# Optimization experiments

Measured on AMD Instinct MI355X. Metric: run time of the kernel, lower is better.

The kernel has to match this reference:

```python
import jax, jax.numpy as jnp
import numpy as np

VOCAB_SIZE = 4096
D_EMBED = 256
BETA = 0.25  # unused: module returns raw commit_loss; beta applied by caller


def setup_inputs() -> dict:
    key = jax.random.key(0)
    k_h, k_e = jax.random.split(key)
    h = jax.random.normal(k_h, (16, D_EMBED, 32, 32), dtype=jnp.float32)
    embedding = jax.random.normal(k_e, (VOCAB_SIZE, D_EMBED), dtype=jnp.float32)
    return {"h": h, "embedding": embedding}


def reference(h, embedding):
    B, C, H, W = h.shape
    h = h.astype(jnp.float32)
    # (B, C, H, W) -> (N, C) with N = B*H*W
    h_flat = jnp.transpose(h, (0, 2, 3, 1)).reshape(-1, C)
    dist = (
        jnp.sum(h_flat * h_flat, axis=1, keepdims=True)
        + jnp.sum(embedding * embedding, axis=1)
        - 2.0 * jnp.einsum("nc,vc->nv", h_flat, embedding)
    )
    indices_flat = jnp.argmin(dist, axis=1)
    indices = indices_flat.reshape(B, H, W)
    # gather codebook vectors and restore (B, C, H, W)
    z_q = jnp.transpose(embedding[indices_flat].reshape(B, H, W, C), (0, 3, 1, 2))
    commit_loss = jnp.mean((h - jax.lax.stop_gradient(z_q)) ** 2)
    # straight-through estimator
    z_q_st = h + jax.lax.stop_gradient(z_q - h)
    return z_q_st, indices, commit_loss
```

## Files before the change

kernel.cpp:

```cpp
#include <hip/hip_runtime.h>

#define D 256
#define VOCAB 4096
#define NTOT 16384
#define N_OUT0 4194304
#define MARGIN 0.95f

typedef _Float16 half8 __attribute__((ext_vector_type(8)));
typedef float f32x4 __attribute__((ext_vector_type(4)));

__device__ __forceinline__ void gld16(const void* g, void* l) {
    __builtin_amdgcn_global_load_lds(
        (const __attribute__((address_space(1))) void*)g,
        (__attribute__((address_space(3))) void*)l, 16, 0, 0);
}

__device__ __forceinline__ unsigned long long pack_key(float d, int v) {
    unsigned u = __float_as_uint(d);
    u ^= ((unsigned)((int)u >> 31)) | 0x80000000u;
    return ((unsigned long long)u << 32) | (unsigned)v;
}

__global__ __launch_bounds__(256) void k_pack(const float* __restrict__ h,
                                              const float* __restrict__ emb,
                                              _Float16* __restrict__ Apk,
                                              _Float16* __restrict__ Bpk,
                                              float* __restrict__ esq) {
    __shared__ float S[16384];
    const int tid = threadIdx.x;
    const int bid = blockIdx.x;
    if (bid < 256) {
        const int bm = bid >> 2, w = bid & 3;
        const int b = bm >> 2, p0 = (bm & 3) << 8;
#pragma unroll 4
        for (int cl = 0; cl < 64; ++cl)
            S[cl * 256 + tid] =
                h[((size_t)b << 18) + ((size_t)(w * 64 + cl) << 10) + (size_t)(p0 + tid)];
        __syncthreads();
        _Float16* dstA = Apk + (size_t)bm * 65536 + (size_t)w * 16384;
#pragma unroll
        for (int kk = 0; kk < 2; ++kk)
#pragma unroll
            for (int q = 0; q < 4; ++q) {
                alignas(16) _Float16 hv[8];
#pragma unroll
                for (int j = 0; j < 8; ++j) hv[j] = (_Float16)S[(kk * 32 + q * 8 + j) * 256 + tid];
                *(half8*)(dstA + (kk * 4 + q) * 2048 + tid * 8) = *(half8*)hv;
            }
    } else {
        const int bn = bid - 256, v0 = bn << 7;
        float eacc = 0.f;
        _Float16* dstB = Bpk + (size_t)bn * 32768;
        const int kk = tid >> 7, r = tid & 127;
        const int sr = (r & 64) + ((r & 15) * 4) + ((r & 63) >> 4);
        for (int w = 0; w < 4; ++w) {
            __syncthreads();
#pragma unroll 4
            for (int i = 0; i < 32; ++i) {
                int rr = i * 4 + (tid >> 6), cc = tid & 63;
                S[rr * 65 + cc] = emb[(size_t)(v0 + rr) * 256 + w * 64 + cc];
            }
            __syncthreads();
            if (tid < 128)
#pragma unroll 4
                for (int cc = 0; cc < 64; ++cc) { float x = S[tid * 65 + cc]; eacc = fmaf(x, x, eacc); }
#pragma unroll
            for (int q = 0; q < 4; ++q) {
                alignas(16) _Float16 ev[8];
#pragma unroll
                for (int j = 0; j < 8; ++j) ev[j] = (_Float16)S[sr * 65 + kk * 32 + q * 8 + j];
                *(half8*)(dstB + w * 8192 + (kk * 4 + q) * 1024 + r * 8) = *(half8*)ev;
            }
        }
        if (tid < 128) esq[v0 + tid] = eacc;
    }
}

__global__ __launch_bounds__(256, 2) void k_gemm(const _Float16* __restrict__ Apk,
                                                 const _Float16* __restrict__ Bpk,
                                                 const float* __restrict__ esq,
                                                 float* __restrict__ top1) {
    __shared__ _Float16 As[16384];
    __shared__ _Float16 Bs[8192];

    const int tid = threadIdx.x;
    const int bn = blockIdx.x >> 6, bm = blockIdx.x & 63;
    const int m0 = bm << 8, n0 = bn << 7;
    const int wv = tid >> 6, l = tid & 63;
    const int wm = wv & 1, wn = wv >> 1;
    const int quad = l >> 4, j16 = l & 15;

    f32x4 acc[8][4];
#pragma unroll
    for (int i = 0; i < 8; ++i)
#pragma unroll
        for (int j = 0; j < 4; ++j) acc[i][j] = (f32x4)0.0f;

    const char* Ag = (const char*)(Apk + (size_t)bm * 65536) + tid * 16;
    const char* Bg = (const char*)(Bpk + (size_t)bn * 32768) + tid * 16;
    _Float16* Asw = As + tid * 8;
    _Float16* Bsw = Bs + tid * 8;
    const _Float16* aB = As + quad * 2048 + (wm * 128 + j16) * 8;
    const _Float16* bB = Bs + quad * 1024 + (wn * 64 + j16) * 8;

    for (int w = 0; w < 4; ++w) {
#pragma unroll
        for (int i = 0; i < 8; ++i) gld16(Ag + w * 32768 + i * 4096, Asw + i * 2048);
#pragma unroll
        for (int i = 0; i < 4; ++i) gld16(Bg + w * 16384 + i * 4096, Bsw + i * 2048);
        __syncthreads();
#pragma unroll
        for (int kk = 0; kk < 2; ++kk) {
            half8 af[8], bf[4];
#pragma unroll
            for (int mt = 0; mt < 8; ++mt) af[mt] = *(const half8*)(aB + kk * 8192 + mt * 128);
#pragma unroll
            for (int nt = 0; nt < 4; ++nt) bf[nt] = *(const half8*)(bB + kk * 4096 + nt * 128);
#pragma unroll
            for (int mt = 0; mt < 8; ++mt)
#pragma unroll
                for (int nt = 0; nt < 4; ++nt)
                    acc[mt][nt] = __builtin_amdgcn_mfma_f32_16x16x32_f16(af[mt], bf[nt], acc[mt][nt], 0, 0, 0);
        }
        __syncthreads();
    }

    const float4 es4 = *(const float4*)(esq + n0 + wn * 64 + j16 * 4);
    const size_t tbase = ((size_t)m0 + wm * 128) * 128 + (unsigned)(bn * 4 + wn * 2 + (j16 >> 3));
#pragma unroll
    for (int mt = 0; mt < 8; ++mt) {
#pragma unroll
        for (int r = 0; r < 4; ++r) {
            float d0 = es4.x - 2.0f * acc[mt][0][r];
            float d1 = es4.y - 2.0f * acc[mt][1][r];
            float d2 = es4.z - 2.0f * acc[mt][2][r];
            float d3 = es4.w - 2.0f * acc[mt][3][r];
            float mn = fminf(fminf(d0, d1), fminf(d2, d3));
            mn = fminf(mn, __shfl_xor(mn, 1, 64));
            mn = fminf(mn, __shfl_xor(mn, 2, 64));
            mn = fminf(mn, __shfl_xor(mn, 4, 64));
            if ((j16 & 7) == 0)
                top1[tbase + (size_t)(mt * 16 + quad * 4 + r) * 128] = mn;
        }
    }
}

__global__ __launch_bounds__(256) void k_refine(const float* __restrict__ h,
                                                const float* __restrict__ emb,
                                                const float* __restrict__ esq,
                                                const float* __restrict__ top1,
                                                unsigned long long* __restrict__ gbest) {
    const int tid = threadIdx.x;
    const int n = blockIdx.x * 4 + (tid >> 6);
    const int l = tid & 63;
    const int b = n >> 10, p = n & 1023;

    const float2 gm = *(const float2*)(top1 + (size_t)n * 128 + l * 2);
    float m1 = fminf(gm.x, gm.y);
#pragma unroll
    for (int m = 32; m >= 1; m >>= 1) m1 = fminf(m1, __shfl_xor(m1, m, 64));
    const float thr = m1 + MARGIN;

    float hreg[4];
#pragma unroll
    for (int i = 0; i < 4; ++i)
        hreg[i] = h[((size_t)b << 18) + ((size_t)(l * 4 + i) << 10) + (size_t)p];

    unsigned long long best = ~0ULL;
#pragma unroll
    for (int j = 0; j < 2; ++j) {
        unsigned long long mask = __ballot((j == 0 ? gm.x : gm.y) <= thr);
        while (mask) {
            const int s = __builtin_ctzll(mask);
            mask &= mask - 1;
            const int g = s * 2 + j;
            const int vg = g << 5;
            for (int t = 0; t < 32; ++t) {
                const int v = vg + t;
                float4 e4 = *(const float4*)(emb + ((size_t)v << 8) + l * 4);
                float part = hreg[0] * e4.x;
                part = fmaf(hreg[1], e4.y, part);
                part = fmaf(hreg[2], e4.z, part);
                part = fmaf(hreg[3], e4.w, part);
#pragma unroll
                for (int m = 32; m >= 1; m >>= 1) part += __shfl_xor(part, m, 64);
                unsigned long long ke = pack_key(esq[v] - 2.0f * part, v);
                best = ke < best ? ke : best;
            }
        }
    }
    if (l == 0) gbest[n] = best;
}

__global__ __launch_bounds__(256) void k_gather(const float* __restrict__ h,
                                                const float* __restrict__ emb,
                                                const unsigned long long* __restrict__ gbest,
                                                float* __restrict__ out0,
                                                float* __restrict__ out1,
                                                float* __restrict__ plsum) {
    __shared__ float zq[32][260];
    __shared__ float wred[4];
    const int tid = threadIdx.x;
    const int lane = tid & 63;
    const int w = tid >> 6;
    const int n0 = blockIdx.x * 32;
    const int b = n0 >> 10;
    const int p0 = n0 & 1023;
#pragma unroll
    for (int rr = 0; rr < 8; ++rr) {
        int r = w * 8 + rr;
        unsigned idx = (unsigned)(gbest[n0 + r] & 0xFFFFFFFFULL);
        float4 e4 = *(const float4*)(emb + (size_t)idx * D + lane * 4);
        *(float4*)&zq[r][lane * 4] = e4;
    }
    if (tid < 32) {
        unsigned idx = (unsigned)(gbest[n0 + tid] & 0xFFFFFFFFULL);
        out1[n0 + tid] = (float)idx;
    }
    __syncthreads();
    float lsum = 0.0f;
    const size_t base = ((size_t)b * D) << 10;
#pragma unroll 4
    for (int it = 0; it < 32; ++it) {
        int c = it * 8 + (tid >> 5);
        int pp = tid & 31;
        float z = zq[pp][c];
        size_t g = base + ((size_t)c << 10) + p0 + pp;
        float hv = h[g];
        out0[g] = hv + (z - hv);
        float d = hv - z;
        lsum = fmaf(d, d, lsum);
    }
#pragma unroll
    for (int m = 32; m >= 1; m >>= 1) lsum += __shfl_xor(lsum, m, 64);
    if (lane == 0) wred[w] = lsum;
    __syncthreads();
    if (tid == 0) plsum[blockIdx.x] = wred[0] + wred[1] + wred[2] + wred[3];
}

__global__ __launch_bounds__(256) void k_fin(const float* __restrict__ plsum,
                                             float* __restrict__ out2) {
    __shared__ float wred[4];
    const int tid = threadIdx.x;
    float s = plsum[tid] + plsum[tid + 256];
#pragma unroll
    for (int m = 32; m >= 1; m >>= 1) s += __shfl_xor(s, m, 64);
    if ((tid & 63) == 0) wred[tid >> 6] = s;
    __syncthreads();
    if (tid == 0) out2[0] = (wred[0] + wred[1] + wred[2] + wred[3]) * (1.0f / (float)N_OUT0);
}

extern "C" void kernel_launch(void* const* d_in, const int* in_sizes, int n_in,
                              void* d_out, int out_size, void* d_ws, size_t ws_size,
                              hipStream_t stream) {
    const float* h = (const float*)d_in[0];
    const float* emb = (const float*)d_in[1];
    float* out0 = (float*)d_out;
    float* out1 = out0 + N_OUT0;
    float* out2 = out1 + NTOT;

    char* w = (char*)d_ws;
    _Float16* Apk = (_Float16*)(w);
    _Float16* Bpk = (_Float16*)(w + 8388608);
    float* top1 = (float*)(w + 10485760);
    float* esq = (float*)(w + 18874368);
    unsigned long long* gbest = (unsigned long long*)(w + 18890752);
    float* plsum = (float*)(w + 19021824);

    hipLaunchKernelGGL(k_pack, dim3(288), dim3(256), 0, stream, h, emb, Apk, Bpk, esq);
    hipLaunchKernelGGL(k_gemm, dim3(2048), dim3(256), 0, stream, Apk, Bpk, esq, top1);
    hipLaunchKernelGGL(k_refine, dim3(4096), dim3(256), 0, stream, h, emb, esq, top1, gbest);
    hipLaunchKernelGGL(k_gather, dim3(NTOT / 32), dim3(256), 0, stream, h, emb, gbest, out0, out1, plsum);
    hipLaunchKernelGGL(k_fin, dim3(1), dim3(256), 0, stream, plsum, out2);
}
```

Baseline: 210.1 us.

## Fuse refine and gather kernels, staging h tile in shared memory

Merges the per-row candidate refinement kernel and the gather/loss kernel into one kernel per 32-position block. The h tile is loaded once into shared memory, reused for the refinement dot products and for the output and loss pass, and the chosen indices stay in shared memory instead of going through a global buffer. This removes a launch, the gbest round-trip and a second strided read of h. The cost is that each block now runs 8 refine rows serially per wave with only 512 blocks, which lowers parallelism for the latency-bound refine loop.

Measured after the change: 244.0 us. +16.1%, slower.

```diff
diff --git a/kernel.cpp b/kernel.cpp
--- a/kernel.cpp
+++ b/kernel.cpp
@@ -145,89 +145,97 @@
     }
 }
 
-__global__ __launch_bounds__(256) void k_refine(const float* __restrict__ h,
+__global__ __launch_bounds__(256) void k_finish(const float* __restrict__ h,
                                                 const float* __restrict__ emb,
                                                 const float* __restrict__ esq,
                                                 const float* __restrict__ top1,
-                                                unsigned long long* __restrict__ gbest) {
-    const int tid = threadIdx.x;
-    const int n = blockIdx.x * 4 + (tid >> 6);
-    const int l = tid & 63;
-    const int b = n >> 10, p = n & 1023;
-
-    const float2 gm = *(const float2*)(top1 + (size_t)n * 128 + l * 2);
-    float m1 = fminf(gm.x, gm.y);
-#pragma unroll
-    for (int m = 32; m >= 1; m >>= 1) m1 = fminf(m1, __shfl_xor(m1, m, 64));
-    const float thr = m1 + MARGIN;
-
-    float hreg[4];
-#pragma unroll
-    for (int i = 0; i < 4; ++i)
-        hreg[i] = h[((size_t)b << 18) + ((size_t)(l * 4 + i) << 10) + (size_t)p];
-
-    unsigned long long best = ~0ULL;
-#pragma unroll
-    for (int j = 0; j < 2; ++j) {
-        unsigned long long mask = __ballot((j == 0 ? gm.x : gm.y) <= thr);
-        while (mask) {
-            const int s = __builtin_ctzll(mask);
-            mask &= mask - 1;
-            const int g = s * 2 + j;
-            const int vg = g << 5;
-            for (int t = 0; t < 32; ++t) {
-                const int v = vg + t;
-                float4 e4 = *(const float4*)(emb + ((size_t)v << 8) + l * 4);
-                float part = hreg[0] * e4.x;
-                part = fmaf(hreg[1], e4.y, part);
-                part = fmaf(hreg[2], e4.z, part);
-                part = fmaf(hreg[3], e4.w, part);
-#pragma unroll
-                for (int m = 32; m >= 1; m >>= 1) part += __shfl_xor(part, m, 64);
-                unsigned long long ke = pack_key(esq[v] - 2.0f * part, v);
-                best = ke < best ? ke : best;
-            }
-        }
-    }
-    if (l == 0) gbest[n] = best;
-}
-
-__global__ __launch_bounds__(256) void k_gather(const float* __restrict__ h,
-                                                const float* __restrict__ emb,
-                                                const unsigned long long* __restrict__ gbest,
                                                 float* __restrict__ out0,
                                                 float* __restrict__ out1,
                                                 float* __restrict__ plsum) {
+    __shared__ float Sh[32][257];
     __shared__ float zq[32][260];
+    __shared__ int idxs[32];
     __shared__ float wred[4];
+
     const int tid = threadIdx.x;
     const int lane = tid & 63;
     const int w = tid >> 6;
     const int n0 = blockIdx.x * 32;
     const int b = n0 >> 10;
     const int p0 = n0 & 1023;
+    const size_t base = (size_t)b << 18;
+
+    {
+        const int pp = tid & 31, c0 = tid >> 5;
+#pragma unroll 4
+        for (int it = 0; it < 32; ++it) {
+            int c = it * 8 + c0;
+            Sh[pp][c] = h[base + ((size_t)c << 10) + (size_t)(p0 + pp)];
+        }
+    }
+    __syncthreads();
+
+#pragma unroll 1
+    for (int rr = 0; rr < 8; ++rr) {
+        const int r = w * 8 + rr;
+        const int n = n0 + r;
+        const float2 gm = *(const float2*)(top1 + ((size_t)n << 7) + lane * 2);
+        float m1 = fminf(gm.x, gm.y);
+#pragma unroll
+        for (int m = 32; m >= 1; m >>= 1) m1 = fminf(m1, __shfl_xor(m1, m, 64));
+        const float thr = m1 + MARGIN;
+
+        const float h0 = Sh[r][lane * 4 + 0];
+        const float h1 = Sh[r][lane * 4 + 1];
+        const float h2 = Sh[r][lane * 4 + 2];
+        const float h3 = Sh[r][lane * 4 + 3];
+
+        unsigned long long best = ~0ULL;
+#pragma unroll
+        for (int j = 0; j < 2; ++j) {
+            unsigned long long mask = __ballot((j == 0 ? gm.x : gm.y) <= thr);
+            while (mask) {
+                const int s = __builtin_ctzll(mask);
+                mask &= mask - 1;
+                const int vg = (s * 2 + j) << 5;
+                for (int t = 0; t < 32; ++t) {
+                    const int v = vg + t;
+                    float4 e4 = *(const float4*)(emb + ((size_t)v << 8) + lane * 4);
+                    float part = h0 * e4.x;
+                    part = fmaf(h1, e4.y, part);
+                    part = fmaf(h2, e4.z, part);
+                    part = fmaf(h3, e4.w, part);
+#pragma unroll
+                    for (int m = 32; m >= 1; m >>= 1) part += __shfl_xor(part, m, 64);
+                    unsigned long long ke = pack_key(esq[v] - 2.0f * part, v);
+                    best = ke < best ? ke : best;
+                }
+            }
+        }
+        if (lane == 0) {
+            const int idx = (int)(best & 0xFFFFFFFFULL);
+            idxs[r] = idx;
+            out1[n] = (float)idx;
+        }
+    }
+    __syncthreads();
+
 #pragma unroll
     for (int rr = 0; rr < 8; ++rr) {
         int r = w * 8 + rr;
-        unsigned idx = (unsigned)(gbest[n0 + r] & 0xFFFFFFFFULL);
-        float4 e4 = *(const float4*)(emb + (size_t)idx * D + lane * 4);
+        float4 e4 = *(const float4*)(emb + ((size_t)idxs[r] << 8) + lane * 4);
         *(float4*)&zq[r][lane * 4] = e4;
     }
-    if (tid < 32) {
-        unsigned idx = (unsigned)(gbest[n0 + tid] & 0xFFFFFFFFULL);
-        out1[n0 + tid] = (float)idx;
-    }
-    __syncthreads();
+    __syncthreads();
+
     float lsum = 0.0f;
-    const size_t base = ((size_t)b * D) << 10;
 #pragma unroll 4
     for (int it = 0; it < 32; ++it) {
         int c = it * 8 + (tid >> 5);
         int pp = tid & 31;
         float z = zq[pp][c];
-        size_t g = base + ((size_t)c << 10) + p0 + pp;
-        float hv = h[g];
-        out0[g] = hv + (z - hv);
+        float hv = Sh[pp][c];
+        out0[base + ((size_t)c << 10) + (size_t)(p0 + pp)] = hv + (z - hv);
         float d = hv - z;
         lsum = fmaf(d, d, lsum);
     }
@@ -264,12 +272,10 @@
     _Float16* Bpk = (_Float16*)(w + 8388608);
     float* top1 = (float*)(w + 10485760);
     float* esq = (float*)(w + 18874368);
-    unsigned long long* gbest = (unsigned long long*)(w + 18890752);
-    float* plsum = (float*)(w + 19021824);
+    float* plsum = (float*)(w + 18890752);
 
     hipLaunchKernelGGL(k_pack, dim3(288), dim3(256), 0, stream, h, emb, Apk, Bpk, esq);
     hipLaunchKernelGGL(k_gemm, dim3(2048), dim3(256), 0, stream, Apk, Bpk, esq, top1);
-    hipLaunchKernelGGL(k_refine, dim3(4096), dim3(256), 0, stream, h, emb, esq, top1, gbest);
-    hipLaunchKernelGGL(k_gather, dim3(NTOT / 32), dim3(256), 0, stream, h, emb, gbest, out0, out1, plsum);
+    hipLaunchKernelGGL(k_finish, dim3(NTOT / 32), dim3(256), 0, stream, h, emb, esq, top1, out0, out1, plsum);
     hipLaunchKernelGGL(k_fin, dim3(1), dim3(256), 0, stream, plsum, out2);
 }
```
